# Kernel tuning notes

Measured on AMD Instinct MI355X. Metric: run time of the kernel, lower is better.

Reference implementation:

```python
import jax, jax.numpy as jnp
import numpy as np

B, S, H, KVH, D = 2, 4096, 32, 8, 64
HID = H * D          # 2048
WIN = 256            # sliding window size (incl. self)
CHK = 128            # chunk size for linear attention
NREP = H // KVH


def setup_inputs() -> dict:
    key = jax.random.key(0)
    ks = jax.random.split(key, 5)
    hidden_states = jax.random.normal(ks[0], (B, S, HID), jnp.float32)
    # RoPE tables (Llama-style)
    inv_freq = 1.0 / (10000.0 ** (jnp.arange(0, D, 2, dtype=jnp.float32) / D))
    freqs = jnp.arange(S, dtype=jnp.float32)[:, None] * inv_freq[None, :]
    emb = jnp.concatenate([freqs, freqs], axis=-1)          # [S, D]
    cos = jnp.broadcast_to(jnp.cos(emb)[None], (B, S, D)).astype(jnp.float32)
    sin = jnp.broadcast_to(jnp.sin(emb)[None], (B, S, D)).astype(jnp.float32)
    scale = 0.02
    Wq = jax.random.normal(ks[1], (HID, HID), jnp.float32) * scale
    Wk = jax.random.normal(ks[2], (KVH * D, HID), jnp.float32) * scale
    Wv = jax.random.normal(ks[3], (KVH * D, HID), jnp.float32) * scale
    Wo = jax.random.normal(ks[4], (HID, HID), jnp.float32) * scale
    return {"hidden_states": hidden_states, "cos": cos, "sin": sin,
            "Wq": Wq, "Wk": Wk, "Wv": Wv, "Wo": Wo}


def rotate_half(x):
    x1, x2 = jnp.split(x, 2, axis=-1)
    return jnp.concatenate([-x2, x1], axis=-1)


def local_window_attention(q, k, v):
    nb = S // WIN
    qb = q.reshape(B, H, nb, WIN, D)
    kb = k.reshape(B, H, nb, WIN, D)
    vb = v.reshape(B, H, nb, WIN, D)
    zpad = jnp.zeros_like(kb[:, :, :1])
    kcat = jnp.concatenate([jnp.concatenate([zpad, kb[:, :, :-1]], axis=2), kb], axis=3)  # [B,H,nb,2W,D]
    vcat = jnp.concatenate([jnp.concatenate([zpad, vb[:, :, :-1]], axis=2), vb], axis=3)
    scores = jnp.einsum('bhnqd,bhnkd->bhnqk', qb, kcat) / jnp.sqrt(jnp.float32(D))
    i = jnp.arange(WIN)[:, None]          # query pos within block
    j = jnp.arange(2 * WIN)[None, :]      # key pos within concat window
    diff = i + WIN - j                    # q_abs - key_abs
    base = (diff >= 0) & (diff < WIN)     # causal + window
    n = jnp.arange(nb)[:, None, None]
    valid = (n * WIN + j[None] - WIN) >= 0   # key_abs >= 0 (mask block-0 padding)
    mask = base[None] & valid                # [nb, W, 2W]
    scores = jnp.where(mask[None, None], scores, -1e30)
    attn = jax.nn.softmax(scores, axis=-1)
    out = jnp.einsum('bhnqk,bhnkd->bhnqd', attn, vcat)
    return out.reshape(B, H, S, D)


def linear_memory_attention(q, k, v):
    # causal linear attention with elu+1 feature map, chunked prefix state
    phi = lambda x: jax.nn.elu(x) + 1.0
    nc = S // CHK
    pq = phi(q).reshape(B, H, nc, CHK, D)
    pk = phi(k).reshape(B, H, nc, CHK, D)
    vc = v.reshape(B, H, nc, CHK, D)
    # intra-chunk (causal within chunk)
    cm = jnp.tril(jnp.ones((CHK, CHK), bool))
    scores = jnp.einsum('bhncd,bhnkd->bhnck', pq, pk)
    scores = jnp.where(cm, scores, 0.0)
    num = jnp.einsum('bhnck,bhnkd->bhncd', scores, vc)
    den = scores.sum(-1)
    # inter-chunk via exclusive prefix sums of KV state
    kv = jnp.einsum('bhnkd,bhnke->bhnde', pk, vc)      # [B,H,nc,D,D]
    ks = pk.sum(axis=3)                                # [B,H,nc,D]
    z4 = jnp.zeros_like(kv[:, :, :1])
    Sprev = jnp.concatenate([z4, jnp.cumsum(kv, axis=2)[:, :, :-1]], axis=2)
    z3 = jnp.zeros_like(ks[:, :, :1])
    zprev = jnp.concatenate([z3, jnp.cumsum(ks, axis=2)[:, :, :-1]], axis=2)
    num = num + jnp.einsum('bhncd,bhnde->bhnce', pq, Sprev)
    den = den + jnp.einsum('bhncd,bhnd->bhnc', pq, zprev)
    out = num / (den[..., None] + 1e-6)
    return out.reshape(B, H, S, D)


def reference(hidden_states, cos, sin, Wq, Wk, Wv, Wo):
    q = jnp.einsum('bsh,oh->bso', hidden_states, Wq).reshape(B, S, H, D).transpose(0, 2, 1, 3)
    k = jnp.einsum('bsh,oh->bso', hidden_states, Wk).reshape(B, S, KVH, D).transpose(0, 2, 1, 3)
    v = jnp.einsum('bsh,oh->bso', hidden_states, Wv).reshape(B, S, KVH, D).transpose(0, 2, 1, 3)
    c = cos[:, None]  # [B,1,S,D]
    s = sin[:, None]
    q = q * c + rotate_half(q) * s
    k = k * c + rotate_half(k) * s
    k = jnp.repeat(k, NREP, axis=1)
    v = jnp.repeat(v, NREP, axis=1)
    local_out = local_window_attention(q, k, v)
    linear_out = linear_memory_attention(q, k, v)
    hybrid = 0.5 * local_out + 0.5 * linear_out              # [B,H,S,D]
    hybrid = hybrid.transpose(0, 2, 1, 3).reshape(B, S, HID)
    return jnp.einsum('bsh,oh->bso', hybrid, Wo)
```

## Files before the change

### kernel.cpp

```cpp
#include <hip/hip_runtime.h>

#define gB 2
#define gS 4096
#define gH 32
#define gKVH 8
#define gHID 2048
#define gNC 32
#define gBS (gB*gS)

using bf16x8 = __attribute__((ext_vector_type(8))) short;
using f32x4  = __attribute__((ext_vector_type(4))) float;

__device__ __forceinline__ float bf2f(unsigned short u){
  return __uint_as_float(((unsigned)u) << 16);
}
__device__ __forceinline__ unsigned short f2bf(float f){
  unsigned u = __float_as_uint(f);
  u = (u + 0x7fffu + ((u >> 16) & 1u)) >> 16;
  return (unsigned short)u;
}
__device__ __forceinline__ float phi_f(float x){ return x > 0.f ? x + 1.f : __expf(x); }

__device__ __forceinline__ void unpack8(uint4 v, unsigned short* o){
  o[0]=(unsigned short)(v.x&0xffffu); o[1]=(unsigned short)(v.x>>16);
  o[2]=(unsigned short)(v.y&0xffffu); o[3]=(unsigned short)(v.y>>16);
  o[4]=(unsigned short)(v.z&0xffffu); o[5]=(unsigned short)(v.z>>16);
  o[6]=(unsigned short)(v.w&0xffffu); o[7]=(unsigned short)(v.w>>16);
}
__device__ __forceinline__ uint4 pack8(const unsigned short* s){
  uint4 v;
  v.x = (unsigned)s[0] | ((unsigned)s[1]<<16);
  v.y = (unsigned)s[2] | ((unsigned)s[3]<<16);
  v.z = (unsigned)s[4] | ((unsigned)s[5]<<16);
  v.w = (unsigned)s[6] | ((unsigned)s[7]<<16);
  return v;
}

typedef const __attribute__((address_space(1))) void* gas_ptr;
typedef __attribute__((address_space(3))) void* las_ptr;
__device__ __forceinline__ void gload16(const void* g, void* l){
  __builtin_amdgcn_global_load_lds((gas_ptr)g, (las_ptr)l, 16, 0, 0);
}

__global__ void cvt_all(const float* __restrict__ hidden, const float* __restrict__ Wq,
                        const float* __restrict__ Wk, const float* __restrict__ Wv,
                        const float* __restrict__ Wo, unsigned short* __restrict__ hbf,
                        unsigned short* __restrict__ wqkv, unsigned short* __restrict__ wob)
{
  const long HG = (long)gBS*gHID/4;
  const long QG = 1048576, KG = 262144, VG = 262144, OG = 1048576;
  const long total = HG + QG + KG + VG + OG;
  long stride = (long)gridDim.x * blockDim.x;
  for (long i = (long)blockIdx.x*blockDim.x + threadIdx.x; i < total; i += stride){
    const float* src; unsigned short* dst; long off;
    if (i < HG)                { src = hidden; dst = hbf;                          off = i; }
    else if (i < HG+QG)        { src = Wq;     dst = wqkv;                         off = i - HG; }
    else if (i < HG+QG+KG)     { src = Wk;     dst = wqkv + (size_t)2048*gHID;     off = i - HG - QG; }
    else if (i < HG+QG+KG+VG)  { src = Wv;     dst = wqkv + (size_t)2560*gHID;     off = i - HG - QG - KG; }
    else                       { src = Wo;     dst = wob;                          off = i - HG - QG - KG - VG; }
    float4 v = *(const float4*)(src + off*4);
    ushort4 o;
    o.x = f2bf(v.x); o.y = f2bf(v.y); o.z = f2bf(v.z); o.w = f2bf(v.w);
    *(ushort4*)(dst + off*4) = o;
  }
}

__global__ __launch_bounds__(512, 2) void gemm_qkv(const unsigned short* __restrict__ A,
                                                   const unsigned short* __restrict__ Bm,
                                                   const float* __restrict__ cosb,
                                                   const float* __restrict__ sinb,
                                                   unsigned short* __restrict__ q_r,
                                                   unsigned short* __restrict__ k_r,
                                                   unsigned short* __restrict__ vproj)
{
  const int Kdim = 2048;
  __shared__ unsigned short Sh[2*24576];
  int tid = threadIdx.x, lane = tid & 63, w = tid >> 6, lr = lane & 15, lg = lane >> 4;
  int wm = w >> 2, wn = w & 3;
  const int ntn = 12;
  int nwg = gridDim.x;
  int bid = (int)blockIdx.x;
  int swz = (bid & 7) * (nwg >> 3) + (bid >> 3);
  long m0 = (long)(swz / ntn) * 128;
  long n0 = (long)(swz % ntn) * 256;
  const int NT = Kdim >> 6;

  f32x4 acc[4][4] = {};

  const char* gsrc[6]; unsigned ldst[6];
  #pragma unroll
  for (int i = 0; i < 2; ++i){
    int c = w*64 + lane + i*512;
    int row = c >> 3, g = c & 7;
    int colb = (g ^ (row & 7)) << 4;
    gsrc[i] = (const char*)A + ((m0 + row) * (long)Kdim)*2 + colb;
    ldst[i] = (unsigned)((w*64 + i*512)*16);
  }
  #pragma unroll
  for (int i = 0; i < 4; ++i){
    int c = w*64 + lane + i*512;
    int row = c >> 3, g = c & 7;
    int colb = (g ^ (row & 7)) << 4;
    gsrc[2+i] = (const char*)Bm + ((n0 + row) * (long)Kdim)*2 + colb;
    ldst[2+i] = (unsigned)(16384 + (w*64 + i*512)*16);
  }
  auto stage = [&](int t){
    int sb = (t & 1) * 49152;
    long kb = (long)t << 7;
    #pragma unroll
    for (int i = 0; i < 6; ++i)
      gload16(gsrc[i] + kb, (char*)Sh + sb + ldst[i]);
  };

  stage(0);
  for (int t = 0; t < NT; ++t){
    asm volatile("s_waitcnt vmcnt(0)" ::: "memory");
    __builtin_amdgcn_s_barrier();
    if (t + 1 < NT) stage(t + 1);
    int sb = (t & 1) * 24576;
    #pragma unroll
    for (int kk = 0; kk < 2; ++kk){
      bf16x8 af[4], bfr[4];
      #pragma unroll
      for (int m = 0; m < 4; ++m){
        int row = wm*64 + m*16 + lr;
        af[m] = *(const bf16x8*)&Sh[sb + row*64 + (((kk*4 + lg) ^ (row & 7)) << 3)];
      }
      #pragma unroll
      for (int n = 0; n < 4; ++n){
        int row = wn*64 + n*16 + lr;
        bfr[n] = *(const bf16x8*)&Sh[sb + 8192 + row*64 + (((kk*4 + lg) ^ (row & 7)) << 3)];
      }
      __builtin_amdgcn_s_setprio(1);
      #pragma unroll
      for (int m = 0; m < 4; ++m)
        #pragma unroll
        for (int n = 0; n < 4; ++n)
          acc[m][n] = __builtin_amdgcn_mfma_f32_16x16x32_bf16(af[m], bfr[n], acc[m][n], 0, 0, 0);
      __builtin_amdgcn_s_setprio(0);
    }
  }

  long colbase = n0 + wn*64;
  if (colbase < 2048){
    int head = (int)(colbase >> 6);
    #pragma unroll
    for (int m = 0; m < 4; ++m)
      #pragma unroll
      for (int r = 0; r < 4; ++r){
        long srow = m0 + wm*64 + m*16 + 4*lg + r;
        int b = (int)(srow >> 12), s = (int)(srow & 4095);
        const float* cp = cosb + srow*64;
        const float* sp = sinb + srow*64;
        unsigned short* op = q_r + ((size_t)(b*gH + head)*gS + s)*64;
        #pragma unroll
        for (int n = 0; n < 2; ++n){
          int d = n*16 + lr;
          float x1 = acc[m][n][r], x2 = acc[m][n+2][r];
          op[d]      = f2bf(x1*cp[d]    - x2*sp[d]);
          op[d+32]   = f2bf(x2*cp[d+32] + x1*sp[d+32]);
        }
      }
  } else if (colbase < 2560){
    int head = (int)(colbase >> 6) - 32;
    #pragma unroll
    for (int m = 0; m < 4; ++m)
      #pragma unroll
      for (int r = 0; r < 4; ++r){
        long srow = m0 + wm*64 + m*16 + 4*lg + r;
        int b = (int)(srow >> 12), s = (int)(srow & 4095);
        const float* cp = cosb + srow*64;
        const float* sp = sinb + srow*64;
        unsigned short* op = k_r + ((size_t)(b*gKVH + head)*gS + s)*64;
        #pragma unroll
        for (int n = 0; n < 2; ++n){
          int d = n*16 + lr;
          float x1 = acc[m][n][r], x2 = acc[m][n+2][r];
          op[d]      = f2bf(x1*cp[d]    - x2*sp[d]);
          op[d+32]   = f2bf(x2*cp[d+32] + x1*sp[d+32]);
        }
      }
  } else {
    #pragma unroll
    for (int m = 0; m < 4; ++m)
      #pragma unroll
      for (int r = 0; r < 4; ++r){
        long srow = m0 + wm*64 + m*16 + 4*lg + r;
        unsigned short* op = vproj + (size_t)srow*512 + (colbase - 2560);
        #pragma unroll
        for (int n = 0; n < 4; ++n)
          op[n*16 + lr] = f2bf(acc[m][n][r]);
      }
  }
}

template<int OUT_BF16>
__global__ __launch_bounds__(512, 2) void gemm256(const unsigned short* __restrict__ A,
                                                  const unsigned short* __restrict__ Bm,
                                                  void* __restrict__ Cout,
                                                  int Mdim, int Ndim, int Kdim)
{
  __shared__ unsigned short Sh[2*32768];
  int tid = threadIdx.x, lane = tid & 63, w = tid >> 6, lr = lane & 15, lg = lane >> 4;
  int wm = w >> 2, wn = w & 3;
  int ntn = Ndim >> 8;
  int nwg = gridDim.x;
  int bid = (int)blockIdx.x;
  int swz = (bid & 7) * (nwg >> 3) + (bid >> 3);
  long m0 = (long)(swz / ntn) * 256;
  long n0 = (long)(swz % ntn) * 256;
  int NT = Kdim >> 6;

  f32x4 acc[8][4] = {};

  const char* gsrc[8]; unsigned ldst[8];
  #pragma unroll
  for (int i = 0; i < 4; ++i){
    int c = w*64 + lane + i*512;
    int row = c >> 3, g = c & 7;
    int colb = (g ^ (row & 7)) << 4;
    gsrc[i]   = (const char*)A  + ((m0 + row) * (long)Kdim)*2 + colb;
    ldst[i]   = (unsigned)((w*64 + i*512)*16);
    gsrc[4+i] = (const char*)Bm + ((n0 + row) * (long)Kdim)*2 + colb;
    ldst[4+i] = (unsigned)(32768 + (w*64 + i*512)*16);
  }
  auto stage = [&](int t){
    int sb = (t & 1) * 65536;
    long kb = (long)t << 7;
    #pragma unroll
    for (int i = 0; i < 8; ++i)
      gload16(gsrc[i] + kb, (char*)Sh + sb + ldst[i]);
  };

  stage(0);
  for (int t = 0; t < NT; ++t){
    asm volatile("s_waitcnt vmcnt(0)" ::: "memory");
    __builtin_amdgcn_s_barrier();
    if (t + 1 < NT) stage(t + 1);
    int sb = (t & 1) * 32768;
    #pragma unroll
    for (int kk = 0; kk < 2; ++kk){
      bf16x8 af[8], bfr[4];
      #pragma unroll
      for (int m = 0; m < 8; ++m){
        int row = wm*128 + m*16 + lr;
        af[m] = *(const bf16x8*)&Sh[sb + row*64 + (((kk*4 + lg) ^ (row & 7)) << 3)];
      }
      #pragma unroll
      for (int n = 0; n < 4; ++n){
        int row = wn*64 + n*16 + lr;
        bfr[n] = *(const bf16x8*)&Sh[sb + 16384 + row*64 + (((kk*4 + lg) ^ (row & 7)) << 3)];
      }
      __builtin_amdgcn_s_setprio(1);
      #pragma unroll
      for (int m = 0; m < 8; ++m)
        #pragma unroll
        for (int n = 0; n < 4; ++n)
          acc[m][n] = __builtin_amdgcn_mfma_f32_16x16x32_bf16(af[m], bfr[n], acc[m][n], 0, 0, 0);
      __builtin_amdgcn_s_setprio(0);
    }
  }

  #pragma unroll
  for (int m = 0; m < 8; ++m)
    #pragma unroll
    for (int n = 0; n < 4; ++n)
      #pragma unroll
      for (int r = 0; r < 4; ++r){
        long row = m0 + wm*128 + m*16 + 4*lg + r;
        long col = n0 + wn*64 + n*16 + lr;
        float v = acc[m][n][r];
        if (OUT_BF16) ((unsigned short*)Cout)[row*Ndim + col] = f2bf(v);
        else          ((float*)Cout)[row*Ndim + col] = v;
      }
}

__global__ __launch_bounds__(256) void transpose2(const unsigned short* __restrict__ k_r,
                                                  unsigned short* __restrict__ ktr,
                                                  const unsigned short* __restrict__ vproj,
                                                  unsigned short* __restrict__ vt)
{
  __shared__ unsigned short T[64*72];
  int bid = blockIdx.x;
  int mode = bid >> 10; bid &= 1023;
  int st = bid & 63; int kvh = (bid >> 6) & 7; int b = bid >> 9;
  int s0 = st*64;
  int tid = threadIdx.x;
  const unsigned short* ip;
  unsigned short* out;
  size_t tokstr;
  if (mode == 0){ ip = k_r + ((size_t)(b*gKVH+kvh)*gS + s0)*64;      out = ktr; tokstr = 64; }
  else          { ip = vproj + (size_t)(b*gS+s0)*512 + kvh*64;       out = vt;  tokstr = 512; }
  #pragma unroll
  for (int i = 0; i < 2; ++i){
    int cc = tid + 256*i; int sl = cc >> 3, ch = cc & 7;
    *(uint4*)&T[sl*72 + ch*8] = *(const uint4*)&ip[(size_t)sl*tokstr + ch*8];
  }
  __syncthreads();
  unsigned short* op = out + ((size_t)(b*gKVH+kvh)*64)*gS;
  #pragma unroll
  for (int i = 0; i < 2; ++i){
    int cc = tid + 256*i; int d = cc >> 3, ch = cc & 7;
    unsigned short t[8];
    #pragma unroll
    for (int u = 0; u < 8; ++u) t[u] = T[(ch*8+u)*72 + d];
    *(uint4*)&op[(size_t)d*gS + s0 + ch*8] = pack8(t);
  }
}

__global__ __launch_bounds__(512) void local_attn(const unsigned short* __restrict__ q_r,
                                                  const unsigned short* __restrict__ k_r,
                                                  const unsigned short* __restrict__ vt,
                                                  unsigned short* __restrict__ olocal)
{
  __shared__ unsigned short Qs[128*72];
  __shared__ unsigned short Ks[2][64*72];
  __shared__ unsigned short VTs[2][64*72];
  __shared__ unsigned short Ps[8*16*72];
  int bid = blockIdx.x;
  int qt = bid & 31; int h = (bid >> 5) & 31; int b = bid >> 10;
  int kvh = h >> 2;
  int q0 = qt*128;
  int tid = threadIdx.x, lane = tid & 63, w = tid >> 6, lr = lane & 15, lg = lane >> 4;
  const unsigned short* qp = q_r + ((size_t)(b*gH  +h  )*gS + q0)*64;
  const unsigned short* kp = k_r + ((size_t)(b*gKVH+kvh)*gS)*64;
  const unsigned short* vp = vt  + ((size_t)(b*gKVH+kvh)*64)*gS;

  #pragma unroll
  for (int i = 0; i < 2; ++i){
    int cc = tid + 512*i; int row = cc >> 3, ch = cc & 7;
    *(uint4*)&Qs[row*72 + ch*8] = *(const uint4*)&qp[row*64 + ch*8];
  }

  int kt0 = (q0 >= 256) ? 0 : ((256 - q0) >> 6);
  int krow = tid >> 3, kch = tid & 7;
  uint4 kreg, vreg;
  {
    int kb = q0 - 256 + kt0*64;
    kreg = *(const uint4*)&kp[(size_t)(kb+krow)*64 + kch*8];
    vreg = *(const uint4*)&vp[(size_t)krow*gS + kb + kch*8];
    *(uint4*)&Ks[0][krow*72 + kch*8]  = kreg;
    *(uint4*)&VTs[0][krow*72 + kch*8] = vreg;
  }

  float psum[4] = {0.f, 0.f, 0.f, 0.f};
  f32x4 accO[4] = {};
  int wq = w*16;

  for (int kt = kt0; kt < 6; ++kt){
    int cur = (kt - kt0) & 1;
    __syncthreads();
    bool more = (kt + 1 < 6);
    if (more){
      int kb2 = q0 - 256 + (kt+1)*64;
      kreg = *(const uint4*)&kp[(size_t)(kb2+krow)*64 + kch*8];
      vreg = *(const uint4*)&vp[(size_t)krow*gS + kb2 + kch*8];
    }

    f32x4 sc[4] = {};
    #pragma unroll
    for (int kk = 0; kk < 64; kk += 32){
      bf16x8 aq = *(const bf16x8*)&Qs[(wq+lr)*72 + kk + 8*lg];
      #pragma unroll
      for (int f = 0; f < 4; ++f){
        bf16x8 bk = *(const bf16x8*)&Ks[cur][(f*16+lr)*72 + kk + 8*lg];
        sc[f] = __builtin_amdgcn_mfma_f32_16x16x32_bf16(aq, bk, sc[f], 0, 0, 0);
      }
    }
    #pragma unroll
    for (int f = 0; f < 4; ++f)
      #pragma unroll
      for (int r = 0; r < 4; ++r){
        int i = wq + 4*lg + r;
        int j = kt*64 + f*16 + lr;
        bool keep = (j > i) && (j <= i + 256);
        float e = __expf(sc[f][r] * 0.125f);
        float p = keep ? e : 0.f;
        psum[r] += p;
        Ps[w*1152 + (4*lg + r)*72 + f*16 + lr] = f2bf(p);
      }
    #pragma unroll
    for (int kk = 0; kk < 64; kk += 32){
      bf16x8 ap = *(const bf16x8*)&Ps[w*1152 + lr*72 + kk + 8*lg];
      #pragma unroll
      for (int dt = 0; dt < 4; ++dt){
        bf16x8 bv = *(const bf16x8*)&VTs[cur][(dt*16+lr)*72 + kk + 8*lg];
        accO[dt] = __builtin_amdgcn_mfma_f32_16x16x32_bf16(ap, bv, accO[dt], 0, 0, 0);
      }
    }
    if (more){
      *(uint4*)&Ks[cur^1][krow*72 + kch*8]  = kreg;
      *(uint4*)&VTs[cur^1][krow*72 + kch*8] = vreg;
    }
  }
  #pragma unroll
  for (int off = 1; off < 16; off <<= 1)
    #pragma unroll
    for (int r = 0; r < 4; ++r) psum[r] += __shfl_xor(psum[r], off);
  #pragma unroll
  for (int dt = 0; dt < 4; ++dt)
    #pragma unroll
    for (int r = 0; r < 4; ++r){
      int s = q0 + wq + 4*lg + r;
      int d = dt*16 + lr;
      float o = accO[dt][r] / psum[r];
      olocal[((size_t)(b*gS+s)*gH + h)*64 + d] = f2bf(0.5f * o);
    }
}

__global__ __launch_bounds__(256) void lin_pass1(const unsigned short* __restrict__ ktr,
                                                 const unsigned short* __restrict__ vt,
                                                 float* __restrict__ kvbuf, float* __restrict__ ksbuf)
{
  __shared__ unsigned short pkT[64*136];
  __shared__ unsigned short vT[64*136];
  int bid = blockIdx.x;
  int c = bid & 31; int kvh = (bid >> 5) & 7; int b = bid >> 8;
  int tid = threadIdx.x, lane = tid & 63, w = tid >> 6, lr = lane & 15, lg = lane >> 4;
  int s0 = c*128;
  const unsigned short* kp = ktr + ((size_t)(b*gKVH+kvh)*64)*gS;
  const unsigned short* vp = vt  + ((size_t)(b*gKVH+kvh)*64)*gS;
  #pragma unroll
  for (int i = 0; i < 4; ++i){
    int cc = tid + 256*i; int d = cc >> 4, ch = cc & 15;
    unsigned short t[8]; unpack8(*(const uint4*)&kp[(size_t)d*gS + s0 + ch*8], t);
    #pragma unroll
    for (int u = 0; u < 8; ++u) t[u] = f2bf(phi_f(bf2f(t[u])));
    *(uint4*)&pkT[d*136 + ch*8] = pack8(t);
    *(uint4*)&vT[d*136 + ch*8]  = *(const uint4*)&vp[(size_t)d*gS + s0 + ch*8];
  }
  __syncthreads();
  f32x4 acc[4] = {};
  #pragma unroll
  for (int kk = 0; kk < 128; kk += 32){
    bf16x8 a = *(const bf16x8*)&pkT[(16*w+lr)*136 + kk + 8*lg];
    #pragma unroll
    for (int et = 0; et < 4; ++et){
      bf16x8 bv = *(const bf16x8*)&vT[(16*et+lr)*136 + kk + 8*lg];
      acc[et] = __builtin_amdgcn_mfma_f32_16x16x32_bf16(a, bv, acc[et], 0, 0, 0);
    }
  }
  size_t base = (size_t)((b*gKVH+kvh)*gNC + c);
  float* kvp = kvbuf + base*4096;
  #pragma unroll
  for (int et = 0; et < 4; ++et)
    #pragma unroll
    for (int r = 0; r < 4; ++r)
      kvp[(16*w + 4*lg + r)*64 + 16*et + lr] = acc[et][r];
  if (tid < 64){
    float sum = 0.f;
    for (int k = 0; k < 128; ++k) sum += bf2f(pkT[tid*136 + k]);
    ksbuf[base*64 + tid] = sum;
  }
}

__global__ void lin_pass2(float* __restrict__ kvbuf, float* __restrict__ ksbuf){
  int t = blockIdx.x*256 + threadIdx.x;
  const int per = 4096 + 64;
  if (t >= gB*gKVH*per) return;
  int bh = t / per; int e = t % per;
  if (e < 4096){
    float* p = kvbuf + (size_t)bh*gNC*4096 + e;
    float acc = 0.f;
    for (int cix = 0; cix < gNC; ++cix){ float v = p[(size_t)cix*4096]; p[(size_t)cix*4096] = acc; acc += v; }
  } else {
    float* p = ksbuf + (size_t)bh*gNC*64 + (e - 4096);
    float acc = 0.f;
    for (int cix = 0; cix < gNC; ++cix){ float v = p[cix*64]; p[cix*64] = acc; acc += v; }
  }
}

__global__ __launch_bounds__(256) void lin_pass3(const unsigned short* __restrict__ q_r,
                                                 const unsigned short* __restrict__ k_r,
                                                 const unsigned short* __restrict__ vt,
                                                 const float* __restrict__ Sprev,
                                                 const float* __restrict__ zprev,
                                                 const unsigned short* __restrict__ olocal,
                                                 unsigned short* __restrict__ hout)
{
  __shared__ unsigned short pq[128*72];
  __shared__ unsigned short pk[64*72];
  __shared__ unsigned short Ph[128*72];
  __shared__ unsigned short vT[64*72];
  __shared__ unsigned short SpT[64*72];
  __shared__ float zp[64];

  int bid = blockIdx.x;
  int c = bid & 31; int h = (bid >> 5) & 31; int b = bid >> 10;
  int kvh = h >> 2;
  int tid = threadIdx.x, lane = tid & 63, w = tid >> 6, lr = lane & 15, lg = lane >> 4;
  int s0 = c*128;
  const unsigned short* qp = q_r + ((size_t)(b*gH  +h  )*gS + s0)*64;
  const unsigned short* kp = k_r + ((size_t)(b*gKVH+kvh)*gS + s0)*64;
  const unsigned short* vp = vt  + ((size_t)(b*gKVH+kvh)*64)*gS;
  const float* Sp  = Sprev + ((size_t)((b*gKVH+kvh)*gNC + c))*4096;
  const float* zpg = zprev + ((size_t)((b*gKVH+kvh)*gNC + c))*64;

  #pragma unroll
  for (int i = 0; i < 4; ++i){
    int cc = tid + 256*i; int row = cc >> 3, d0 = (cc & 7)*8;
    unsigned short t[8]; unpack8(*(const uint4*)(qp + row*64 + d0), t);
    #pragma unroll
    for (int u = 0; u < 8; ++u) t[u] = f2bf(phi_f(bf2f(t[u])));
    *(uint4*)&pq[row*72 + d0] = pack8(t);
  }
  #pragma unroll
  for (int i = 0; i < 16; ++i){
    int f = tid + 256*i; int d = f >> 6, e = f & 63;
    SpT[e*72 + d] = f2bf(Sp[f]);
  }
  if (tid < 64) zp[tid] = zpg[tid];

  float den[2][4] = {};
  f32x4 accO[2][4] = {};

  for (int kh = 0; kh < 2; ++kh){
    __syncthreads();
    #pragma unroll
    for (int i = 0; i < 2; ++i){
      int cc = tid + 256*i; int kr = cc >> 3, d0 = (cc & 7)*8;
      unsigned short t[8]; unpack8(*(const uint4*)(kp + (kh*64+kr)*64 + d0), t);
      #pragma unroll
      for (int u = 0; u < 8; ++u) t[u] = f2bf(phi_f(bf2f(t[u])));
      *(uint4*)&pk[kr*72 + d0] = pack8(t);
      *(uint4*)&vT[kr*72 + d0] = *(const uint4*)&vp[(size_t)kr*gS + s0 + kh*64 + d0];
    }
    __syncthreads();

    f32x4 sc[2][4] = {};
    #pragma unroll
    for (int kk = 0; kk < 64; kk += 32){
      bf16x8 a[2];
      #pragma unroll
      for (int rt = 0; rt < 2; ++rt) a[rt] = *(const bf16x8*)&pq[(32*w+16*rt+lr)*72 + kk + 8*lg];
      #pragma unroll
      for (int ct = 0; ct < 4; ++ct){
        bf16x8 bk = *(const bf16x8*)&pk[(16*ct+lr)*72 + kk + 8*lg];
        #pragma unroll
        for (int rt = 0; rt < 2; ++rt)
          sc[rt][ct] = __builtin_amdgcn_mfma_f32_16x16x32_bf16(a[rt], bk, sc[rt][ct], 0, 0, 0);
      }
    }
    #pragma unroll
    for (int rt = 0; rt < 2; ++rt)
      #pragma unroll
      for (int ct = 0; ct < 4; ++ct)
        #pragma unroll
        for (int r = 0; r < 4; ++r){
          int qrow = 32*w + 16*rt + 4*lg + r;
          int krow = kh*64 + 16*ct + lr;
          float sv = (krow <= qrow) ? sc[rt][ct][r] : 0.f;
          den[rt][r] += sv;
          Ph[qrow*72 + 16*ct + lr] = f2bf(sv);
        }
    #pragma unroll
    for (int kk = 0; kk < 64; kk += 32){
      bf16x8 ap[2];
      #pragma unroll
      for (int rt = 0; rt < 2; ++rt) ap[rt] = *(const bf16x8*)&Ph[(32*w+16*rt+lr)*72 + kk + 8*lg];
      #pragma unroll
      for (int et = 0; et < 4; ++et){
        bf16x8 bv = *(const bf16x8*)&vT[(16*et+lr)*72 + kk + 8*lg];
        #pragma unroll
        for (int rt = 0; rt < 2; ++rt)
          accO[rt][et] = __builtin_amdgcn_mfma_f32_16x16x32_bf16(ap[rt], bv, accO[rt][et], 0, 0, 0);
      }
    }
  }
  #pragma unroll
  for (int kk = 0; kk < 64; kk += 32){
    bf16x8 a[2];
    #pragma unroll
    for (int rt = 0; rt < 2; ++rt) a[rt] = *(const bf16x8*)&pq[(32*w+16*rt+lr)*72 + kk + 8*lg];
    #pragma unroll
    for (int et = 0; et < 4; ++et){
      bf16x8 bs = *(const bf16x8*)&SpT[(16*et+lr)*72 + kk + 8*lg];
      #pragma unroll
      for (int rt = 0; rt < 2; ++rt)
        accO[rt][et] = __builtin_amdgcn_mfma_f32_16x16x32_bf16(a[rt], bs, accO[rt][et], 0, 0, 0);
    }
  }
  #pragma unroll
  for (int rt = 0; rt < 2; ++rt)
    #pragma unroll
    for (int r = 0; r < 4; ++r){
      int qrow = 32*w + 16*rt + 4*lg + r;
      float part = 0.f;
      #pragma unroll
      for (int u = 0; u < 4; ++u){
        int d = 4*lr + u;
        part += bf2f(pq[qrow*72 + d]) * zp[d];
      }
      den[rt][r] += part;
      #pragma unroll
      for (int off = 1; off < 16; off <<= 1)
        den[rt][r] += __shfl_xor(den[rt][r], off);
    }
  #pragma unroll
  for (int rt = 0; rt < 2; ++rt)
    #pragma unroll
    for (int et = 0; et < 4; ++et)
      #pragma unroll
      for (int r = 0; r < 4; ++r){
        int qrow = 32*w + 16*rt + 4*lg + r;
        int e = 16*et + lr;
        float o = accO[rt][et][r] / (den[rt][r] + 1e-6f);
        int s = s0 + qrow;
        size_t idx = ((size_t)(b*gS+s)*gH + h)*64 + e;
        hout[idx] = f2bf(bf2f(olocal[idx]) + 0.5f * o);
      }
}

extern "C" void kernel_launch(void* const* d_in, const int* in_sizes, int n_in,
                              void* d_out, int out_size, void* d_ws, size_t ws_size,
                              hipStream_t stream)
{
  const float* hidden = (const float*)d_in[0];
  const float* cosb   = (const float*)d_in[1];
  const float* sinb   = (const float*)d_in[2];
  const float* Wq     = (const float*)d_in[3];
  const float* Wk     = (const float*)d_in[4];
  const float* Wv     = (const float*)d_in[5];
  const float* Wo     = (const float*)d_in[6];
  float* out = (float*)d_out;

  char* ws = (char*)d_ws;
  size_t off = 0;
  auto alloc = [&](size_t bytes)->void*{
    void* p = ws + off; off += (bytes + 255) & ~(size_t)255; return p;
  };
  unsigned short* hbf    = (unsigned short*)alloc((size_t)gBS*gHID*2);
  unsigned short* wqkv   = (unsigned short*)alloc((size_t)3072*gHID*2);
  unsigned short* wob    = (unsigned short*)alloc((size_t)gHID*gHID*2);
  unsigned short* vproj  = (unsigned short*)alloc((size_t)gBS*512*2);
  unsigned short* q_r    = (unsigned short*)alloc((size_t)gBS*gHID*2);
  unsigned short* k_r    = (unsigned short*)alloc((size_t)gBS*512*2);
  unsigned short* ktr    = (unsigned short*)alloc((size_t)gBS*512*2);
  unsigned short* vt     = (unsigned short*)alloc((size_t)gBS*512*2);
  unsigned short* olocal = (unsigned short*)alloc((size_t)gBS*gHID*2);
  float* kvbuf           = (float*)alloc((size_t)gB*gKVH*gNC*4096*4);
  float* ksbuf           = (float*)alloc((size_t)gB*gKVH*gNC*64*4);

  cvt_all<<<dim3(2048), dim3(256), 0, stream>>>(hidden, Wq, Wk, Wv, Wo, hbf, wqkv, wob);

  gemm_qkv<<<dim3(64*12), dim3(512), 0, stream>>>(hbf, wqkv, cosb, sinb, q_r, k_r, vproj);

  transpose2<<<dim3(2048), dim3(256), 0, stream>>>(k_r, ktr, vproj, vt);

  local_attn<<<dim3(gB*gH*32), dim3(512), 0, stream>>>(q_r, k_r, vt, olocal);
  lin_pass1<<<dim3(gB*gKVH*gNC), dim3(256), 0, stream>>>(ktr, vt, kvbuf, ksbuf);
  lin_pass2<<<dim3((gB*gKVH*(4096+64) + 255)/256), dim3(256), 0, stream>>>(kvbuf, ksbuf);
  lin_pass3<<<dim3(gB*gH*gNC), dim3(256), 0, stream>>>(q_r, k_r, vt, kvbuf, ksbuf, olocal, hbf);

  gemm256<0><<<dim3(32*8), dim3(512), 0, stream>>>(hbf, wob, (void*)out, 8192, 2048, 2048);
}
```

Baseline: 328.7 us.

## Fuse local window attention with linear attention pass3 into one kernel

Merges the sliding-window softmax kernel and the linear-attention intra-chunk/prefix kernel into one kernel per (batch, head, 128-query tile). It reuses the Q tile and the last two K/V tiles already resident in shared memory from the local loop, and drops the intermediate olocal buffer write and read. Shared memory buffers are aliased to hold the phi-transformed Q and the intra-chunk scores. The cost is a longer kernel with more register pressure, and launch bounds now request two blocks per CU.

```diff
diff --git a/kernel.cpp b/kernel.cpp
--- a/kernel.cpp
+++ b/kernel.cpp
@@ -308,15 +308,18 @@
   }
 }
 
-__global__ __launch_bounds__(512) void local_attn(const unsigned short* __restrict__ q_r,
-                                                  const unsigned short* __restrict__ k_r,
-                                                  const unsigned short* __restrict__ vt,
-                                                  unsigned short* __restrict__ olocal)
+__global__ __launch_bounds__(512, 2) void attn_fused(const unsigned short* __restrict__ q_r,
+                                                     const unsigned short* __restrict__ k_r,
+                                                     const unsigned short* __restrict__ vt,
+                                                     const float* __restrict__ Sprev,
+                                                     const float* __restrict__ zprev,
+                                                     unsigned short* __restrict__ hout)
 {
-  __shared__ unsigned short Qs[128*72];
+  __shared__ unsigned short QsPh[128*72];
   __shared__ unsigned short Ks[2][64*72];
   __shared__ unsigned short VTs[2][64*72];
-  __shared__ unsigned short Ps[8*16*72];
+  __shared__ unsigned short Pq[128*72];
+  __shared__ float zp[64];
   int bid = blockIdx.x;
   int qt = bid & 31; int h = (bid >> 5) & 31; int b = bid >> 10;
   int kvh = h >> 2;
@@ -325,11 +328,13 @@
   const unsigned short* qp = q_r + ((size_t)(b*gH  +h  )*gS + q0)*64;
   const unsigned short* kp = k_r + ((size_t)(b*gKVH+kvh)*gS)*64;
   const unsigned short* vp = vt  + ((size_t)(b*gKVH+kvh)*64)*gS;
+  const float* Sp  = Sprev + ((size_t)((b*gKVH+kvh)*gNC + qt))*4096;
+  const float* zpg = zprev + ((size_t)((b*gKVH+kvh)*gNC + qt))*64;
 
   #pragma unroll
   for (int i = 0; i < 2; ++i){
     int cc = tid + 512*i; int row = cc >> 3, ch = cc & 7;
-    *(uint4*)&Qs[row*72 + ch*8] = *(const uint4*)&qp[row*64 + ch*8];
+    *(uint4*)&QsPh[row*72 + ch*8] = *(const uint4*)&qp[row*64 + ch*8];
   }
 
   int kt0 = (q0 >= 256) ? 0 : ((256 - q0) >> 6);
@@ -360,7 +365,7 @@
     f32x4 sc[4] = {};
     #pragma unroll
     for (int kk = 0; kk < 64; kk += 32){
-      bf16x8 aq = *(const bf16x8*)&Qs[(wq+lr)*72 + kk + 8*lg];
+      bf16x8 aq = *(const bf16x8*)&QsPh[(wq+lr)*72 + kk + 8*lg];
       #pragma unroll
       for (int f = 0; f < 4; ++f){
         bf16x8 bk = *(const bf16x8*)&Ks[cur][(f*16+lr)*72 + kk + 8*lg];
@@ -377,11 +382,11 @@
         float e = __expf(sc[f][r] * 0.125f);
         float p = keep ? e : 0.f;
         psum[r] += p;
-        Ps[w*1152 + (4*lg + r)*72 + f*16 + lr] = f2bf(p);
+        Pq[w*1152 + (4*lg + r)*72 + f*16 + lr] = f2bf(p);
       }
     #pragma unroll
     for (int kk = 0; kk < 64; kk += 32){
-      bf16x8 ap = *(const bf16x8*)&Ps[w*1152 + lr*72 + kk + 8*lg];
+      bf16x8 ap = *(const bf16x8*)&Pq[w*1152 + lr*72 + kk + 8*lg];
       #pragma unroll
       for (int dt = 0; dt < 4; ++dt){
         bf16x8 bv = *(const bf16x8*)&VTs[cur][(dt*16+lr)*72 + kk + 8*lg];
@@ -398,13 +403,110 @@
     #pragma unroll
     for (int r = 0; r < 4; ++r) psum[r] += __shfl_xor(psum[r], off);
   #pragma unroll
+  for (int r = 0; r < 4; ++r){
+    float inv = 0.5f / psum[r];
+    #pragma unroll
+    for (int dt = 0; dt < 4; ++dt) accO[dt][r] *= inv;
+  }
+
+  __syncthreads();
+  {
+    int row = tid >> 2, c0 = (tid & 3) * 16;
+    #pragma unroll
+    for (int hlf = 0; hlf < 2; ++hlf){
+      unsigned short t[8];
+      unpack8(*(const uint4*)&QsPh[row*72 + c0 + hlf*8], t);
+      #pragma unroll
+      for (int u = 0; u < 8; ++u) t[u] = f2bf(phi_f(bf2f(t[u])));
+      *(uint4*)&Pq[row*72 + c0 + hlf*8] = pack8(t);
+    }
+    #pragma unroll
+    for (int bf = 0; bf < 2; ++bf){
+      unsigned short t[8];
+      unpack8(*(const uint4*)&Ks[bf][krow*72 + kch*8], t);
+      #pragma unroll
+      for (int u = 0; u < 8; ++u) t[u] = f2bf(phi_f(bf2f(t[u])));
+      *(uint4*)&Ks[bf][krow*72 + kch*8] = pack8(t);
+    }
+  }
+  __syncthreads();
+
+  float den[4] = {};
+  f32x4 accL[4] = {};
+  #pragma unroll
+  for (int kh = 0; kh < 2; ++kh){
+    int kb = (kt0 + kh) & 1;
+    f32x4 sc[4] = {};
+    #pragma unroll
+    for (int kk = 0; kk < 64; kk += 32){
+      bf16x8 a = *(const bf16x8*)&Pq[(wq+lr)*72 + kk + 8*lg];
+      #pragma unroll
+      for (int ct = 0; ct < 4; ++ct){
+        bf16x8 bk = *(const bf16x8*)&Ks[kb][(16*ct+lr)*72 + kk + 8*lg];
+        sc[ct] = __builtin_amdgcn_mfma_f32_16x16x32_bf16(a, bk, sc[ct], 0, 0, 0);
+      }
+    }
+    #pragma unroll
+    for (int ct = 0; ct < 4; ++ct)
+      #pragma unroll
+      for (int r = 0; r < 4; ++r){
+        int qrow = wq + 4*lg + r;
+        int kro  = kh*64 + 16*ct + lr;
+        float sv = (kro <= qrow) ? sc[ct][r] : 0.f;
+        den[r] += sv;
+        QsPh[qrow*72 + 16*ct + lr] = f2bf(sv);
+      }
+    #pragma unroll
+    for (int kk = 0; kk < 64; kk += 32){
+      bf16x8 ap = *(const bf16x8*)&QsPh[(wq+lr)*72 + kk + 8*lg];
+      #pragma unroll
+      for (int et = 0; et < 4; ++et){
+        bf16x8 bv = *(const bf16x8*)&VTs[kb][(16*et+lr)*72 + kk + 8*lg];
+        accL[et] = __builtin_amdgcn_mfma_f32_16x16x32_bf16(ap, bv, accL[et], 0, 0, 0);
+      }
+    }
+  }
+
+  __syncthreads();
+  #pragma unroll
+  for (int i = 0; i < 8; ++i){
+    int f = tid + 512*i; int d = f >> 6, e = f & 63;
+    QsPh[e*72 + d] = f2bf(Sp[f]);
+  }
+  if (tid < 64) zp[tid] = zpg[tid];
+  __syncthreads();
+  #pragma unroll
+  for (int kk = 0; kk < 64; kk += 32){
+    bf16x8 a = *(const bf16x8*)&Pq[(wq+lr)*72 + kk + 8*lg];
+    #pragma unroll
+    for (int et = 0; et < 4; ++et){
+      bf16x8 bs = *(const bf16x8*)&QsPh[(16*et+lr)*72 + kk + 8*lg];
+      accL[et] = __builtin_amdgcn_mfma_f32_16x16x32_bf16(a, bs, accL[et], 0, 0, 0);
+    }
+  }
+  #pragma unroll
+  for (int r = 0; r < 4; ++r){
+    int qrow = wq + 4*lg + r;
+    float part = 0.f;
+    #pragma unroll
+    for (int u = 0; u < 4; ++u){
+      int d = 4*lr + u;
+      part += bf2f(Pq[qrow*72 + d]) * zp[d];
+    }
+    den[r] += part;
+    #pragma unroll
+    for (int off = 1; off < 16; off <<= 1)
+      den[r] += __shfl_xor(den[r], off);
+  }
+
+  #pragma unroll
   for (int dt = 0; dt < 4; ++dt)
     #pragma unroll
     for (int r = 0; r < 4; ++r){
       int s = q0 + wq + 4*lg + r;
       int d = dt*16 + lr;
-      float o = accO[dt][r] / psum[r];
-      olocal[((size_t)(b*gS+s)*gH + h)*64 + d] = f2bf(0.5f * o);
+      float val = accO[dt][r] + 0.5f * accL[dt][r] / (den[r] + 1e-6f);
+      hout[((size_t)(b*gS+s)*gH + h)*64 + d] = f2bf(val);
     }
 }
 
@@ -470,147 +572,6 @@
   }
 }
 
-__global__ __launch_bounds__(256) void lin_pass3(const unsigned short* __restrict__ q_r,
-                                                 const unsigned short* __restrict__ k_r,
-                                                 const unsigned short* __restrict__ vt,
-                                                 const float* __restrict__ Sprev,
-                                                 const float* __restrict__ zprev,
-                                                 const unsigned short* __restrict__ olocal,
-                                                 unsigned short* __restrict__ hout)
-{
-  __shared__ unsigned short pq[128*72];
-  __shared__ unsigned short pk[64*72];
-  __shared__ unsigned short Ph[128*72];
-  __shared__ unsigned short vT[64*72];
-  __shared__ unsigned short SpT[64*72];
-  __shared__ float zp[64];
-
-  int bid = blockIdx.x;
-  int c = bid & 31; int h = (bid >> 5) & 31; int b = bid >> 10;
-  int kvh = h >> 2;
-  int tid = threadIdx.x, lane = tid & 63, w = tid >> 6, lr = lane & 15, lg = lane >> 4;
-  int s0 = c*128;
-  const unsigned short* qp = q_r + ((size_t)(b*gH  +h  )*gS + s0)*64;
-  const unsigned short* kp = k_r + ((size_t)(b*gKVH+kvh)*gS + s0)*64;
-  const unsigned short* vp = vt  + ((size_t)(b*gKVH+kvh)*64)*gS;
-  const float* Sp  = Sprev + ((size_t)((b*gKVH+kvh)*gNC + c))*4096;
-  const float* zpg = zprev + ((size_t)((b*gKVH+kvh)*gNC + c))*64;
-
-  #pragma unroll
-  for (int i = 0; i < 4; ++i){
-    int cc = tid + 256*i; int row = cc >> 3, d0 = (cc & 7)*8;
-    unsigned short t[8]; unpack8(*(const uint4*)(qp + row*64 + d0), t);
-    #pragma unroll
-    for (int u = 0; u < 8; ++u) t[u] = f2bf(phi_f(bf2f(t[u])));
-    *(uint4*)&pq[row*72 + d0] = pack8(t);
-  }
-  #pragma unroll
-  for (int i = 0; i < 16; ++i){
-    int f = tid + 256*i; int d = f >> 6, e = f & 63;
-    SpT[e*72 + d] = f2bf(Sp[f]);
-  }
-  if (tid < 64) zp[tid] = zpg[tid];
-
-  float den[2][4] = {};
-  f32x4 accO[2][4] = {};
-
-  for (int kh = 0; kh < 2; ++kh){
-    __syncthreads();
-    #pragma unroll
-    for (int i = 0; i < 2; ++i){
-      int cc = tid + 256*i; int kr = cc >> 3, d0 = (cc & 7)*8;
-      unsigned short t[8]; unpack8(*(const uint4*)(kp + (kh*64+kr)*64 + d0), t);
-      #pragma unroll
-      for (int u = 0; u < 8; ++u) t[u] = f2bf(phi_f(bf2f(t[u])));
-      *(uint4*)&pk[kr*72 + d0] = pack8(t);
-      *(uint4*)&vT[kr*72 + d0] = *(const uint4*)&vp[(size_t)kr*gS + s0 + kh*64 + d0];
-    }
-    __syncthreads();
-
-    f32x4 sc[2][4] = {};
-    #pragma unroll
-    for (int kk = 0; kk < 64; kk += 32){
-      bf16x8 a[2];
-      #pragma unroll
-      for (int rt = 0; rt < 2; ++rt) a[rt] = *(const bf16x8*)&pq[(32*w+16*rt+lr)*72 + kk + 8*lg];
-      #pragma unroll
-      for (int ct = 0; ct < 4; ++ct){
-        bf16x8 bk = *(const bf16x8*)&pk[(16*ct+lr)*72 + kk + 8*lg];
-        #pragma unroll
-        for (int rt = 0; rt < 2; ++rt)
-          sc[rt][ct] = __builtin_amdgcn_mfma_f32_16x16x32_bf16(a[rt], bk, sc[rt][ct], 0, 0, 0);
-      }
-    }
-    #pragma unroll
-    for (int rt = 0; rt < 2; ++rt)
-      #pragma unroll
-      for (int ct = 0; ct < 4; ++ct)
-        #pragma unroll
-        for (int r = 0; r < 4; ++r){
-          int qrow = 32*w + 16*rt + 4*lg + r;
-          int krow = kh*64 + 16*ct + lr;
-          float sv = (krow <= qrow) ? sc[rt][ct][r] : 0.f;
-          den[rt][r] += sv;
-          Ph[qrow*72 + 16*ct + lr] = f2bf(sv);
-        }
-    #pragma unroll
-    for (int kk = 0; kk < 64; kk += 32){
-      bf16x8 ap[2];
-      #pragma unroll
-      for (int rt = 0; rt < 2; ++rt) ap[rt] = *(const bf16x8*)&Ph[(32*w+16*rt+lr)*72 + kk + 8*lg];
-      #pragma unroll
-      for (int et = 0; et < 4; ++et){
-        bf16x8 bv = *(const bf16x8*)&vT[(16*et+lr)*72 + kk + 8*lg];
-        #pragma unroll
-        for (int rt = 0; rt < 2; ++rt)
-          accO[rt][et] = __builtin_amdgcn_mfma_f32_16x16x32_bf16(ap[rt], bv, accO[rt][et], 0, 0, 0);
-      }
-    }
-  }
-  #pragma unroll
-  for (int kk = 0; kk < 64; kk += 32){
-    bf16x8 a[2];
-    #pragma unroll
-    for (int rt = 0; rt < 2; ++rt) a[rt] = *(const bf16x8*)&pq[(32*w+16*rt+lr)*72 + kk + 8*lg];
-    #pragma unroll
-    for (int et = 0; et < 4; ++et){
-      bf16x8 bs = *(const bf16x8*)&SpT[(16*et+lr)*72 + kk + 8*lg];
-      #pragma unroll
-      for (int rt = 0; rt < 2; ++rt)
-        accO[rt][et] = __builtin_amdgcn_mfma_f32_16x16x32_bf16(a[rt], bs, accO[rt][et], 0, 0, 0);
-    }
-  }
-  #pragma unroll
-  for (int rt = 0; rt < 2; ++rt)
-    #pragma unroll
-    for (int r = 0; r < 4; ++r){
-      int qrow = 32*w + 16*rt + 4*lg + r;
-      float part = 0.f;
-      #pragma unroll
-      for (int u = 0; u < 4; ++u){
-        int d = 4*lr + u;
-        part += bf2f(pq[qrow*72 + d]) * zp[d];
-      }
-      den[rt][r] += part;
-      #pragma unroll
-      for (int off = 1; off < 16; off <<= 1)
-        den[rt][r] += __shfl_xor(den[rt][r], off);
-    }
-  #pragma unroll
-  for (int rt = 0; rt < 2; ++rt)
-    #pragma unroll
-    for (int et = 0; et < 4; ++et)
-      #pragma unroll
-      for (int r = 0; r < 4; ++r){
-        int qrow = 32*w + 16*rt + 4*lg + r;
-        int e = 16*et + lr;
-        float o = accO[rt][et][r] / (den[rt][r] + 1e-6f);
-        int s = s0 + qrow;
-        size_t idx = ((size_t)(b*gS+s)*gH + h)*64 + e;
-        hout[idx] = f2bf(bf2f(olocal[idx]) + 0.5f * o);
-      }
-}
-
 extern "C" void kernel_launch(void* const* d_in, const int* in_sizes, int n_in,
                               void* d_out, int out_size, void* d_ws, size_t ws_size,
                               hipStream_t stream)
@@ -637,7 +598,6 @@
   unsigned short* k_r    = (unsigned short*)alloc((size_t)gBS*512*2);
   unsigned short* ktr    = (unsigned short*)alloc((size_t)gBS*512*2);
   unsigned short* vt     = (unsigned short*)alloc((size_t)gBS*512*2);
-  unsigned short* olocal = (unsigned short*)alloc((size_t)gBS*gHID*2);
   float* kvbuf           = (float*)alloc((size_t)gB*gKVH*gNC*4096*4);
   float* ksbuf           = (float*)alloc((size_t)gB*gKVH*gNC*64*4);
 
@@ -647,10 +607,10 @@
 
   transpose2<<<dim3(2048), dim3(256), 0, stream>>>(k_r, ktr, vproj, vt);
 
-  local_attn<<<dim3(gB*gH*32), dim3(512), 0, stream>>>(q_r, k_r, vt, olocal);
   lin_pass1<<<dim3(gB*gKVH*gNC), dim3(256), 0, stream>>>(ktr, vt, kvbuf, ksbuf);
   lin_pass2<<<dim3((gB*gKVH*(4096+64) + 255)/256), dim3(256), 0, stream>>>(kvbuf, ksbuf);
-  lin_pass3<<<dim3(gB*gH*gNC), dim3(256), 0, stream>>>(q_r, k_r, vt, kvbuf, ksbuf, olocal, hbf);
+
+  attn_fused<<<dim3(gB*gH*32), dim3(512), 0, stream>>>(q_r, k_r, vt, kvbuf, ksbuf, hbf);
 
   gemm256<0><<<dim3(32*8), dim3(512), 0, stream>>>(hbf, wob, (void*)out, 8192, 2048, 2048);
 }
```

Measured after the change: 316.0 us. -3.9%, faster.
